# Kernel optimization log

Measured on AMD Instinct MI355X. Metric: run time of the kernel, lower is better.

The kernel has to match this reference:

```python
import jax, jax.numpy as jnp
import numpy as np

B, N, L = 4, 16, 2048
E = 32768
CH = (64, 128, 128, 128)
EPS = 1e-5


def setup_inputs() -> dict:
    key = jax.random.key(0)
    ks = jax.random.split(key, 6)
    x = jax.random.normal(ks[0], (B, N, CH[0], L), jnp.float32)
    edge_index = jax.random.randint(ks[1], (2, E), 0, L, dtype=jnp.int64)

    def xavier(k, fi, fo):
        std = (2.0 / (fi + fo)) ** 0.5
        return jax.random.normal(k, (fi, fo), jnp.float32) * std

    W1 = xavier(ks[2], CH[0], CH[1])
    W2 = xavier(ks[3], 2 * CH[1], CH[2])
    W3 = xavier(ks[4], 2 * CH[2], CH[3])
    return dict(
        x=x, edge_index=edge_index,
        W1=W1, b1=jnp.zeros((CH[1],), jnp.float32),
        W2=W2, b2=jnp.zeros((CH[2],), jnp.float32),
        W3=W3, b3=jnp.zeros((CH[3],), jnp.float32),
        g1=jnp.ones((2 * CH[1],), jnp.float32), be1=jnp.zeros((2 * CH[1],), jnp.float32),
        g2=jnp.ones((2 * CH[2],), jnp.float32), be2=jnp.zeros((2 * CH[2],), jnp.float32),
        g3=jnp.ones((2 * CH[3],), jnp.float32), be3=jnp.zeros((2 * CH[3],), jnp.float32),
    )


def _gcn_norm(edge_index, l):
    # PyG gcn_norm with improved=True: self loops get weight 2, sym normalization
    src, dst = edge_index[0], edge_index[1]
    loop = jnp.arange(l)
    src_f = jnp.concatenate([src, loop])
    dst_f = jnp.concatenate([dst, loop])
    w = jnp.concatenate([jnp.ones((src.shape[0],), jnp.float32),
                         2.0 * jnp.ones((l,), jnp.float32)])
    deg = jax.ops.segment_sum(w, dst_f, num_segments=l)
    dinv = jnp.where(deg > 0, jax.lax.rsqrt(deg), 0.0)
    return src_f, dst_f, dinv[src_f] * w * dinv[dst_f]


def _gcn(h, W, bias, src, dst, norm):
    # h: [G, l, c_in] -> [G, l, c_out];  out[i] = sum_{j->i} norm_ij * (h_j @ W) + b
    hW = jnp.einsum('glc,cf->glf', h, W)
    msg = hW[:, src, :] * norm[None, :, None]
    out = jnp.zeros_like(hW).at[:, dst, :].add(msg)
    return out + bias


def _block(h, W, bias, g, beta, src, dst, norm, b, n, l):
    # h: [b, n, l, c_in]
    a = _gcn(h.reshape(b * n, l, h.shape[-1]), W, bias, src, dst, norm)
    a = a.reshape(b, n, l, -1)
    amax = a.max(axis=1, keepdims=True)
    a = jnp.concatenate([a, jnp.broadcast_to(amax, a.shape)], axis=-1)  # [b,n,l,2c]
    # BatchNorm1d training stats over (b, n, l) per channel (biased var)
    mean = a.mean(axis=(0, 1, 2))
    var = a.var(axis=(0, 1, 2))
    return jax.nn.relu((a - mean) * jax.lax.rsqrt(var + EPS) * g + beta)


def reference(x, edge_index, W1, b1, W2, b2, W3, b3, g1, be1, g2, be2, g3, be3):
    b, n, c, l = x.shape
    h = jnp.transpose(x, (0, 1, 3, 2))  # [b, n, l, c] node-major
    src, dst, norm = _gcn_norm(edge_index, l)
    h = _block(h, W1, b1, g1, be1, src, dst, norm, b, n, l)
    h = _block(h, W2, b2, g2, be2, src, dst, norm, b, n, l)
    h = _block(h, W3, b3, g3, be3, src, dst, norm, b, n, l)
    # match torch output layout [b*n, 2*channels[3], l]
    return jnp.transpose(h.reshape(b * n, l, -1), (0, 2, 1))
```

## Files before the change

kernel.cpp:

```cpp
#include <hip/hip_runtime.h>
#include <hip/hip_bf16.h>
#include <cstddef>
#include <cstdint>

#define BB 4
#define NN 16
#define GG 64
#define LL 2048
#define EE 32768
#define EF (EE + LL)
#define C0 64
#define CC 256
#define EPS 1e-5f

typedef __bf16 bf16x8 __attribute__((ext_vector_type(8)));
typedef __bf16 bf16x4 __attribute__((ext_vector_type(4)));
typedef __bf16 bf16x2 __attribute__((ext_vector_type(2)));
typedef float f32x4 __attribute__((ext_vector_type(4)));

struct __align__(8) Edge { int col; float val; };


__global__ void detect_kernel(const int* __restrict__ ei, int* __restrict__ flag) {
    int t = threadIdx.x;
    int bad = 0;
    for (int i = t; i < 256; i += 64) bad |= (ei[2 * i + 1] != 0) ? 1 : 0;
    int any = __any(bad);
    if (t == 0) *flag = any ? 0 : 1;
}

__global__ void convert_kernel(const void* __restrict__ ei, const int* __restrict__ flag,
                               int* __restrict__ e32) {
    int i = blockIdx.x * 256 + threadIdx.x;
    if (i >= 2 * EE) return;
    int v;
    if (*flag)
        v = (int)((const long long*)ei)[i];
    else
        v = ((const int*)ei)[i];
    e32[i] = v;
}

__global__ void initdeg_kernel(float* __restrict__ deg, int* __restrict__ cnt) {
    int i = blockIdx.x * 256 + threadIdx.x;
    if (i < LL) { deg[i] = 2.0f; cnt[i] = 1; }
}

__global__ void deg_kernel(const int* __restrict__ e32, float* __restrict__ deg,
                           int* __restrict__ cnt) {
    int e = blockIdx.x * 256 + threadIdx.x;
    if (e >= EE) return;
    int d = e32[EE + e];
    atomicAdd(&deg[d], 1.0f);
    atomicAdd(&cnt[d], 1);
}

__global__ void dinv_kernel(const float* __restrict__ deg, float* __restrict__ dinv) {
    int i = blockIdx.x * 256 + threadIdx.x;
    if (i < LL) dinv[i] = rsqrtf(deg[i]);
}

__global__ void scan_kernel(const int* __restrict__ cnt, int* __restrict__ rowptr,
                            int* __restrict__ cursor) {
    __shared__ int part[256];
    int t = threadIdx.x;
    int base = t * 8;
    int loc[8];
    int s = 0;
#pragma unroll
    for (int j = 0; j < 8; ++j) { loc[j] = s; s += cnt[base + j]; }
    part[t] = s;
    __syncthreads();
    if (t == 0) {
        int run = 0;
        for (int i = 0; i < 256; ++i) { int v = part[i]; part[i] = run; run += v; }
    }
    __syncthreads();
    int off = part[t];
#pragma unroll
    for (int j = 0; j < 8; ++j) {
        int rp = off + loc[j];
        rowptr[base + j] = rp;
        cursor[base + j] = rp;
    }
    if (t == 255) rowptr[LL] = off + s;
}

__global__ void fill_kernel(const int* __restrict__ e32, const float* __restrict__ dinv,
                            int* __restrict__ cursor, Edge* __restrict__ edges) {
    int idx = blockIdx.x * 256 + threadIdx.x;
    if (idx >= EF) return;
    int s, d; float w;
    if (idx < EE) {
        s = e32[idx]; d = e32[EE + idx];
        w = dinv[s] * dinv[d];
    } else {
        int i = idx - EE;
        s = i; d = i;
        w = 2.0f * dinv[i] * dinv[i];
    }
    int pos = atomicAdd(&cursor[d], 1);
    edges[pos].col = s;
    edges[pos].val = w;
}


__global__ void prep_w(const float* __restrict__ W, __bf16* __restrict__ Wf, int K) {
    int t = blockIdx.x * 256 + threadIdx.x;
    int total = (K / 32) * 8 * 64;
    if (t >= total) return;
    int lane = t & 63;
    int rest = t >> 6;
    int n16 = rest & 7;
    int ks = rest >> 3;
    int col = n16 * 16 + (lane & 15);
    int k0 = ks * 32 + (lane >> 4) * 8;
    bf16x8 v;
#pragma unroll
    for (int j = 0; j < 8; ++j) v[j] = (__bf16)W[(size_t)(k0 + j) * 128 + col];
    *(bf16x8*)(Wf + (size_t)t * 8) = v;
}


__global__ void transpose_x(const float* __restrict__ x, float* __restrict__ h) {
    __shared__ float t[32][33];
    int g = blockIdx.z, c0 = blockIdx.y * 32, l0 = blockIdx.x * 32;
    int tx = threadIdx.x, ty = threadIdx.y;
    const float* xp = x + ((size_t)g * C0 + c0) * LL + l0;
#pragma unroll
    for (int i = ty; i < 32; i += 8) t[i][tx] = xp[(size_t)i * LL + tx];
    __syncthreads();
    float* hp = h + ((size_t)g * LL + l0) * C0 + c0;
#pragma unroll
    for (int i = ty; i < 32; i += 8) hp[(size_t)i * C0 + tx] = t[tx][i];
}


template <int K, bool BN>
__global__ __launch_bounds__(256) void gemm_mfma(const float* __restrict__ A0,
                                                 const float* __restrict__ amax,
                                                 const float* __restrict__ scb,
                                                 const __bf16* __restrict__ Wf,
                                                 __bf16* __restrict__ hw) {
    const int g = blockIdx.y;
    const int l0 = blockIdx.x * 64;
    const int tid = threadIdx.x;
    const int wid = tid >> 6;
    const int lane = tid & 63;
    __shared__ __align__(16) __bf16 As[64 * 64];

    f32x4 acc[8];
#pragma unroll
    for (int nf = 0; nf < 8; ++nf) acc[nf] = (f32x4){0.f, 0.f, 0.f, 0.f};

    const int AS = BN ? 128 : 64;

    for (int kt = 0; kt < K / 64; ++kt) {
#pragma unroll
        for (int it = 0; it < 4; ++it) {
            int f4 = tid + it * 256;
            int row = f4 >> 4;
            int kq = (f4 & 15) * 4;
            int gk = kt * 64 + kq;
            float4 v;
            if constexpr (BN) {
                if (gk < 128)
                    v = *(const float4*)(A0 + ((size_t)g * LL + l0 + row) * 128 + gk);
                else
                    v = *(const float4*)(amax + ((size_t)(g >> 4) * LL + l0 + row) * 128 + (gk - 128));
                float4 s = *(const float4*)(scb + gk);
                float4 b = *(const float4*)(scb + 256 + gk);
                v.x = fmaxf(fmaf(v.x, s.x, b.x), 0.f);
                v.y = fmaxf(fmaf(v.y, s.y, b.y), 0.f);
                v.z = fmaxf(fmaf(v.z, s.z, b.z), 0.f);
                v.w = fmaxf(fmaf(v.w, s.w, b.w), 0.f);
            } else {
                v = *(const float4*)(A0 + ((size_t)g * LL + l0 + row) * 64 + gk);
            }
            int sidx = row * 64 + (kq ^ ((row & 7) << 3));
            bf16x4 pv = {(__bf16)v.x, (__bf16)v.y, (__bf16)v.z, (__bf16)v.w};
            *(bf16x4*)(&As[sidx]) = pv;
        }
        __syncthreads();
#pragma unroll
        for (int ks2 = 0; ks2 < 2; ++ks2) {
            const int row = wid * 16 + (lane & 15);
            const int kk = ks2 * 32 + (lane >> 4) * 8;
            bf16x8 af = *(const bf16x8*)(&As[row * 64 + (kk ^ ((row & 7) << 3))]);
            const int ksg = kt * 2 + ks2;
            const __bf16* wp = Wf + (size_t)ksg * 8 * 512 + lane * 8;
#pragma unroll
            for (int nf = 0; nf < 8; ++nf) {
                bf16x8 bfr = *(const bf16x8*)(wp + nf * 512);
                acc[nf] = __builtin_amdgcn_mfma_f32_16x16x32_bf16(af, bfr, acc[nf], 0, 0, 0);
            }
        }
        __syncthreads();
    }
    __bf16* op = hw + ((size_t)g * LL + l0) * 128;
#pragma unroll
    for (int nf = 0; nf < 8; ++nf) {
        int col = nf * 16 + (lane & 15);
#pragma unroll
        for (int j = 0; j < 4; ++j) {
            int row = wid * 16 + (lane >> 4) * 4 + j;
            op[(size_t)row * 128 + col] = (__bf16)acc[nf][j];
        }
    }
}


__global__ __launch_bounds__(256) void agg_kernel(const __bf16* __restrict__ hw,
                                                  const float* __restrict__ bias,
                                                  const int* __restrict__ rowptr,
                                                  const Edge* __restrict__ edges,
                                                  float* __restrict__ aout) {
    const int lane = threadIdx.x & 63;
    int node = blockIdx.x * 4 + (threadIdx.x >> 6);
    node = __builtin_amdgcn_readfirstlane(node);
    const int g = node >> 11, l = node & (LL - 1);
    const __bf16* __restrict__ base = hw + (size_t)g * LL * 128;
    const int j0 = rowptr[l];
    const int deg = rowptr[l + 1] - j0;

    float2 acc = *(const float2*)(bias + 2 * lane);

    for (int d0 = 0; d0 < deg; d0 += 64) {
        const int cnt = min(64, deg - d0);
        Edge e;
        e.col = 0; e.val = 0.0f;
        if (lane < cnt) e = edges[j0 + d0 + lane];
        int d = 0;
        for (; d + 4 <= cnt; d += 4) {
            int c0 = __shfl(e.col, d);
            int c1 = __shfl(e.col, d + 1);
            int c2 = __shfl(e.col, d + 2);
            int c3 = __shfl(e.col, d + 3);
            float w0 = __shfl(e.val, d);
            float w1 = __shfl(e.val, d + 1);
            float w2 = __shfl(e.val, d + 2);
            float w3 = __shfl(e.val, d + 3);
            bf16x2 v0 = *(const bf16x2*)(base + (size_t)c0 * 128 + 2 * lane);
            bf16x2 v1 = *(const bf16x2*)(base + (size_t)c1 * 128 + 2 * lane);
            bf16x2 v2 = *(const bf16x2*)(base + (size_t)c2 * 128 + 2 * lane);
            bf16x2 v3 = *(const bf16x2*)(base + (size_t)c3 * 128 + 2 * lane);
            acc.x = fmaf(w0, (float)v0[0], acc.x); acc.y = fmaf(w0, (float)v0[1], acc.y);
            acc.x = fmaf(w1, (float)v1[0], acc.x); acc.y = fmaf(w1, (float)v1[1], acc.y);
            acc.x = fmaf(w2, (float)v2[0], acc.x); acc.y = fmaf(w2, (float)v2[1], acc.y);
            acc.x = fmaf(w3, (float)v3[0], acc.x); acc.y = fmaf(w3, (float)v3[1], acc.y);
        }
        for (; d < cnt; ++d) {
            int c = __shfl(e.col, d);
            float wv = __shfl(e.val, d);
            bf16x2 v = *(const bf16x2*)(base + (size_t)c * 128 + 2 * lane);
            acc.x = fmaf(wv, (float)v[0], acc.x);
            acc.y = fmaf(wv, (float)v[1], acc.y);
        }
    }
    *(float2*)(aout + (size_t)node * 128 + 2 * lane) = acc;
}


__global__ void maxstats_kernel(const float* __restrict__ a, float* __restrict__ amax,
                                float* __restrict__ sums, float* __restrict__ sumsq) {
    int bb = blockIdx.x >> 7;
    int lt = blockIdx.x & 127;
    int l0 = lt * 16;
    int f = threadIdx.x;
    float s = 0.f, ss = 0.f, sa = 0.f, ssa = 0.f;
    for (int li = 0; li < 16; ++li) {
        int l = l0 + li;
        float m = -3.402823466e38f;
#pragma unroll
        for (int n = 0; n < NN; ++n) {
            float v = a[(((size_t)(bb * NN + n) * LL + l) * 128) + f];
            m = fmaxf(m, v);
            s += v;
            ss = fmaf(v, v, ss);
        }
        amax[((size_t)bb * LL + l) * 128 + f] = m;
        sa += m;
        ssa = fmaf(m, m, ssa);
    }
    atomicAdd(&sums[f], s);
    atomicAdd(&sumsq[f], ss);
    atomicAdd(&sums[128 + f], sa);
    atomicAdd(&sumsq[128 + f], ssa);
}

__global__ void bnfinal_kernel(const float* __restrict__ sums, const float* __restrict__ sumsq,
                               const float* __restrict__ gamma, const float* __restrict__ beta,
                               float* __restrict__ scb) {
    int f = threadIdx.x;
    float cntv = (f < 128) ? (float)(BB * NN * LL) : (float)(BB * LL);
    float mean = sums[f] / cntv;
    float var = sumsq[f] / cntv - mean * mean;
    float s = gamma[f] * rsqrtf(var + EPS);
    scb[f] = s;
    scb[256 + f] = beta[f] - mean * s;
}


__global__ void transpose_norm_out(const float* __restrict__ a, const float* __restrict__ amax,
                                   const float* __restrict__ scb, float* __restrict__ out) {
    __shared__ float t[32][33];
    int g = blockIdx.z, f0 = blockIdx.y * 32, l0 = blockIdx.x * 32;
    int tx = threadIdx.x, ty = threadIdx.y;
    int f = f0 + tx;
    float s = scb[f], b = scb[256 + f];
#pragma unroll
    for (int i = ty; i < 32; i += 8) {
        int l = l0 + i;
        float v;
        if (f0 < 128)
            v = a[((size_t)g * LL + l) * 128 + f];
        else
            v = amax[((size_t)(g >> 4) * LL + l) * 128 + (f - 128)];
        t[i][tx] = fmaxf(fmaf(v, s, b), 0.f);
    }
    __syncthreads();
    float* op = out + ((size_t)g * CC + f0) * LL + l0;
#pragma unroll
    for (int i = ty; i < 32; i += 8) op[(size_t)i * LL + tx] = t[tx][i];
}


extern "C" void kernel_launch(void* const* d_in, const int* in_sizes, int n_in,
                              void* d_out, int out_size, void* d_ws, size_t ws_size,
                              hipStream_t stream) {
    const float* x = (const float*)d_in[0];
    const void* ei = d_in[1];
    const float* W[3] = {(const float*)d_in[2], (const float*)d_in[4], (const float*)d_in[6]};
    const float* bia[3] = {(const float*)d_in[3], (const float*)d_in[5], (const float*)d_in[7]};
    const float* gam[3] = {(const float*)d_in[8], (const float*)d_in[10], (const float*)d_in[12]};
    const float* bet[3] = {(const float*)d_in[9], (const float*)d_in[11], (const float*)d_in[13]};
    float* out = (float*)d_out;

    char* w = (char*)d_ws;
    float* h0   = (float*)w;  w += (size_t)GG * LL * C0 * 4;
    float* a    = (float*)w;  w += (size_t)GG * LL * 128 * 4;
    __bf16* hw  = (__bf16*)w; w += (size_t)GG * LL * 128 * 2;
    float* amax = (float*)w;  w += (size_t)BB * LL * 128 * 4;
    __bf16* Wf[3];
    Wf[0] = (__bf16*)w; w += 65536 * 2;
    Wf[1] = (__bf16*)w; w += 65536 * 2;
    Wf[2] = (__bf16*)w; w += 65536 * 2;
    int*   e32   = (int*)w;    w += (size_t)2 * EE * 4;
    float* deg   = (float*)w;  w += LL * 4;
    int*   cnt   = (int*)w;    w += LL * 4;
    int*   rowptr= (int*)w;    w += (LL + 4) * 4;
    int*   cursor= (int*)w;    w += LL * 4;
    Edge*  edges = (Edge*)w;   w += (size_t)EF * 8;
    float* dinv  = (float*)w;  w += LL * 4;
    float* sums  = (float*)w;  w += 256 * 4;
    float* sumsq = (float*)w;  w += 256 * 4;
    float* scb   = (float*)w;  w += 512 * 4;
    int*   flag  = (int*)w;    w += 256;

    detect_kernel<<<1, 64, 0, stream>>>((const int*)ei, flag);
    convert_kernel<<<(2 * EE + 255) / 256, 256, 0, stream>>>(ei, flag, e32);
    initdeg_kernel<<<(LL + 255) / 256, 256, 0, stream>>>(deg, cnt);
    deg_kernel<<<(EE + 255) / 256, 256, 0, stream>>>(e32, deg, cnt);
    dinv_kernel<<<(LL + 255) / 256, 256, 0, stream>>>(deg, dinv);
    scan_kernel<<<1, 256, 0, stream>>>(cnt, rowptr, cursor);
    fill_kernel<<<(EF + 255) / 256, 256, 0, stream>>>(e32, dinv, cursor, edges);

    prep_w<<<(1024 + 255) / 256, 256, 0, stream>>>(W[0], Wf[0], 64);
    prep_w<<<(4096 + 255) / 256, 256, 0, stream>>>(W[1], Wf[1], 256);
    prep_w<<<(4096 + 255) / 256, 256, 0, stream>>>(W[2], Wf[2], 256);

    transpose_x<<<dim3(LL / 32, C0 / 32, GG), dim3(32, 8), 0, stream>>>(x, h0);

    gemm_mfma<64, false><<<dim3(LL / 64, GG), 256, 0, stream>>>(h0, amax, scb, Wf[0], hw);
    agg_kernel<<<GG * LL / 4, 256, 0, stream>>>(hw, bia[0], rowptr, edges, a);
    hipMemsetAsync(sums, 0, 2 * 256 * 4, stream);
    maxstats_kernel<<<BB * (LL / 16), 128, 0, stream>>>(a, amax, sums, sumsq);
    bnfinal_kernel<<<1, 256, 0, stream>>>(sums, sumsq, gam[0], bet[0], scb);

    gemm_mfma<256, true><<<dim3(LL / 64, GG), 256, 0, stream>>>(a, amax, scb, Wf[1], hw);
    agg_kernel<<<GG * LL / 4, 256, 0, stream>>>(hw, bia[1], rowptr, edges, a);
    hipMemsetAsync(sums, 0, 2 * 256 * 4, stream);
    maxstats_kernel<<<BB * (LL / 16), 128, 0, stream>>>(a, amax, sums, sumsq);
    bnfinal_kernel<<<1, 256, 0, stream>>>(sums, sumsq, gam[1], bet[1], scb);

    gemm_mfma<256, true><<<dim3(LL / 64, GG), 256, 0, stream>>>(a, amax, scb, Wf[2], hw);
    agg_kernel<<<GG * LL / 4, 256, 0, stream>>>(hw, bia[2], rowptr, edges, a);
    hipMemsetAsync(sums, 0, 2 * 256 * 4, stream);
    maxstats_kernel<<<BB * (LL / 16), 128, 0, stream>>>(a, amax, sums, sumsq);
    bnfinal_kernel<<<1, 256, 0, stream>>>(sums, sumsq, gam[2], bet[2], scb);

    transpose_norm_out<<<dim3(LL / 32, CC / 32, GG), dim3(32, 8), 0, stream>>>(a, amax, scb, out);
}
```

Baseline: 597.4 us.

## Vectorize aggregation gathers, fuse setup kernels, drop memsets, enlarge output transpose tiles

The aggregation kernel now has each 16-lane group gather a full 128-channel row with 16-byte bf16x8 loads, four neighbours per step, then reduce the partial sums across the groups with xor shuffles. Several small setup kernels are merged (convert+initdeg, scan+dinv), and the per-layer memsets are removed: the stats buffers are zeroed in the prep kernel and by bnfinal after it reads them. The output transpose moves to 64x64 tiles. This trims launch overhead and gather instruction count, at the cost of extra cross-lane reductions and wasted work when a node's degree is not a multiple of four.

```diff
diff --git a/kernel.cpp b/kernel.cpp
--- a/kernel.cpp
+++ b/kernel.cpp
@@ -29,21 +29,20 @@
     if (t == 0) *flag = any ? 0 : 1;
 }
 
-__global__ void convert_kernel(const void* __restrict__ ei, const int* __restrict__ flag,
-                               int* __restrict__ e32) {
+__global__ void prep_init_kernel(const void* __restrict__ ei, const int* __restrict__ flag,
+                                 int* __restrict__ e32, float* __restrict__ deg,
+                                 int* __restrict__ cnt, float* __restrict__ sums) {
     int i = blockIdx.x * 256 + threadIdx.x;
-    if (i >= 2 * EE) return;
-    int v;
-    if (*flag)
-        v = (int)((const long long*)ei)[i];
-    else
-        v = ((const int*)ei)[i];
-    e32[i] = v;
-}
-
-__global__ void initdeg_kernel(float* __restrict__ deg, int* __restrict__ cnt) {
-    int i = blockIdx.x * 256 + threadIdx.x;
+    if (i < 2 * EE) {
+        int v;
+        if (*flag)
+            v = (int)((const long long*)ei)[i];
+        else
+            v = ((const int*)ei)[i];
+        e32[i] = v;
+    }
     if (i < LL) { deg[i] = 2.0f; cnt[i] = 1; }
+    if (i < 512) sums[i] = 0.0f;
 }
 
 __global__ void deg_kernel(const int* __restrict__ e32, float* __restrict__ deg,
@@ -55,20 +54,19 @@
     atomicAdd(&cnt[d], 1);
 }
 
-__global__ void dinv_kernel(const float* __restrict__ deg, float* __restrict__ dinv) {
-    int i = blockIdx.x * 256 + threadIdx.x;
-    if (i < LL) dinv[i] = rsqrtf(deg[i]);
-}
-
-__global__ void scan_kernel(const int* __restrict__ cnt, int* __restrict__ rowptr,
-                            int* __restrict__ cursor) {
+__global__ void scan_dinv_kernel(const int* __restrict__ cnt, const float* __restrict__ deg,
+                                 int* __restrict__ rowptr, int* __restrict__ cursor,
+                                 float* __restrict__ dinv) {
     __shared__ int part[256];
     int t = threadIdx.x;
     int base = t * 8;
     int loc[8];
     int s = 0;
 #pragma unroll
-    for (int j = 0; j < 8; ++j) { loc[j] = s; s += cnt[base + j]; }
+    for (int j = 0; j < 8; ++j) {
+        loc[j] = s; s += cnt[base + j];
+        dinv[base + j] = rsqrtf(deg[base + j]);
+    }
     part[t] = s;
     __syncthreads();
     if (t == 0) {
@@ -152,8 +150,6 @@
     f32x4 acc[8];
 #pragma unroll
     for (int nf = 0; nf < 8; ++nf) acc[nf] = (f32x4){0.f, 0.f, 0.f, 0.f};
-
-    const int AS = BN ? 128 : 64;
 
     for (int kt = 0; kt < K / 64; ++kt) {
 #pragma unroll
@@ -216,14 +212,18 @@
                                                   const Edge* __restrict__ edges,
                                                   float* __restrict__ aout) {
     const int lane = threadIdx.x & 63;
+    const int grp = lane >> 4;
+    const int ch16 = lane & 15;
     int node = blockIdx.x * 4 + (threadIdx.x >> 6);
     node = __builtin_amdgcn_readfirstlane(node);
     const int g = node >> 11, l = node & (LL - 1);
-    const __bf16* __restrict__ base = hw + (size_t)g * LL * 128;
+    const __bf16* __restrict__ base = hw + (size_t)g * LL * 128 + ch16 * 8;
     const int j0 = rowptr[l];
     const int deg = rowptr[l + 1] - j0;
 
-    float2 acc = *(const float2*)(bias + 2 * lane);
+    float acc[8];
+#pragma unroll
+    for (int j = 0; j < 8; ++j) acc[j] = 0.0f;
 
     for (int d0 = 0; d0 < deg; d0 += 64) {
         const int cnt = min(64, deg - d0);
@@ -231,33 +231,39 @@
         e.col = 0; e.val = 0.0f;
         if (lane < cnt) e = edges[j0 + d0 + lane];
         int d = 0;
-        for (; d + 4 <= cnt; d += 4) {
-            int c0 = __shfl(e.col, d);
-            int c1 = __shfl(e.col, d + 1);
-            int c2 = __shfl(e.col, d + 2);
-            int c3 = __shfl(e.col, d + 3);
-            float w0 = __shfl(e.val, d);
-            float w1 = __shfl(e.val, d + 1);
-            float w2 = __shfl(e.val, d + 2);
-            float w3 = __shfl(e.val, d + 3);
-            bf16x2 v0 = *(const bf16x2*)(base + (size_t)c0 * 128 + 2 * lane);
-            bf16x2 v1 = *(const bf16x2*)(base + (size_t)c1 * 128 + 2 * lane);
-            bf16x2 v2 = *(const bf16x2*)(base + (size_t)c2 * 128 + 2 * lane);
-            bf16x2 v3 = *(const bf16x2*)(base + (size_t)c3 * 128 + 2 * lane);
-            acc.x = fmaf(w0, (float)v0[0], acc.x); acc.y = fmaf(w0, (float)v0[1], acc.y);
-            acc.x = fmaf(w1, (float)v1[0], acc.x); acc.y = fmaf(w1, (float)v1[1], acc.y);
-            acc.x = fmaf(w2, (float)v2[0], acc.x); acc.y = fmaf(w2, (float)v2[1], acc.y);
-            acc.x = fmaf(w3, (float)v3[0], acc.x); acc.y = fmaf(w3, (float)v3[1], acc.y);
-        }
-        for (; d < cnt; ++d) {
-            int c = __shfl(e.col, d);
-            float wv = __shfl(e.val, d);
-            bf16x2 v = *(const bf16x2*)(base + (size_t)c * 128 + 2 * lane);
-            acc.x = fmaf(wv, (float)v[0], acc.x);
-            acc.y = fmaf(wv, (float)v[1], acc.y);
-        }
-    }
-    *(float2*)(aout + (size_t)node * 128 + 2 * lane) = acc;
+        for (; d + 8 <= cnt; d += 8) {
+            int i1 = d + grp, i2 = d + 4 + grp;
+            int c1 = __shfl(e.col, i1); float w1 = __shfl(e.val, i1);
+            int c2 = __shfl(e.col, i2); float w2 = __shfl(e.val, i2);
+            bf16x8 v1 = *(const bf16x8*)(base + (size_t)c1 * 128);
+            bf16x8 v2 = *(const bf16x8*)(base + (size_t)c2 * 128);
+#pragma unroll
+            for (int j = 0; j < 8; ++j) acc[j] = fmaf(w1, (float)v1[j], acc[j]);
+#pragma unroll
+            for (int j = 0; j < 8; ++j) acc[j] = fmaf(w2, (float)v2[j], acc[j]);
+        }
+        for (; d < cnt; d += 4) {
+            int i1 = d + grp;
+            int c1 = __shfl(e.col, i1); float w1 = __shfl(e.val, i1);
+            bf16x8 v1 = *(const bf16x8*)(base + (size_t)c1 * 128);
+#pragma unroll
+            for (int j = 0; j < 8; ++j) acc[j] = fmaf(w1, (float)v1[j], acc[j]);
+        }
+    }
+#pragma unroll
+    for (int j = 0; j < 8; ++j) {
+        acc[j] += __shfl_xor(acc[j], 16);
+        acc[j] += __shfl_xor(acc[j], 32);
+    }
+    if (grp == 0) {
+        float4 b0 = *(const float4*)(bias + ch16 * 8);
+        float4 b1 = *(const float4*)(bias + ch16 * 8 + 4);
+        float4 s0 = make_float4(acc[0] + b0.x, acc[1] + b0.y, acc[2] + b0.z, acc[3] + b0.w);
+        float4 s1 = make_float4(acc[4] + b1.x, acc[5] + b1.y, acc[6] + b1.z, acc[7] + b1.w);
+        float* op = aout + (size_t)node * 128 + ch16 * 8;
+        *(float4*)op = s0;
+        *(float4*)(op + 4) = s1;
+    }
 }
 
 
@@ -288,7 +294,7 @@
     atomicAdd(&sumsq[128 + f], ssa);
 }
 
-__global__ void bnfinal_kernel(const float* __restrict__ sums, const float* __restrict__ sumsq,
+__global__ void bnfinal_kernel(float* __restrict__ sums, float* __restrict__ sumsq,
                                const float* __restrict__ gamma, const float* __restrict__ beta,
                                float* __restrict__ scb) {
     int f = threadIdx.x;
@@ -298,18 +304,20 @@
     float s = gamma[f] * rsqrtf(var + EPS);
     scb[f] = s;
     scb[256 + f] = beta[f] - mean * s;
+    sums[f] = 0.0f;
+    sumsq[f] = 0.0f;
 }
 
 
 __global__ void transpose_norm_out(const float* __restrict__ a, const float* __restrict__ amax,
                                    const float* __restrict__ scb, float* __restrict__ out) {
-    __shared__ float t[32][33];
-    int g = blockIdx.z, f0 = blockIdx.y * 32, l0 = blockIdx.x * 32;
+    __shared__ float t[64][65];
+    int g = blockIdx.z, f0 = blockIdx.y * 64, l0 = blockIdx.x * 64;
     int tx = threadIdx.x, ty = threadIdx.y;
     int f = f0 + tx;
     float s = scb[f], b = scb[256 + f];
 #pragma unroll
-    for (int i = ty; i < 32; i += 8) {
+    for (int i = ty; i < 64; i += 8) {
         int l = l0 + i;
         float v;
         if (f0 < 128)
@@ -321,7 +329,7 @@
     __syncthreads();
     float* op = out + ((size_t)g * CC + f0) * LL + l0;
 #pragma unroll
-    for (int i = ty; i < 32; i += 8) op[(size_t)i * LL + tx] = t[tx][i];
+    for (int i = ty; i < 64; i += 8) op[(size_t)i * LL + tx] = t[tx][i];
 }
 
 
@@ -358,11 +366,9 @@
     int*   flag  = (int*)w;    w += 256;
 
     detect_kernel<<<1, 64, 0, stream>>>((const int*)ei, flag);
-    convert_kernel<<<(2 * EE + 255) / 256, 256, 0, stream>>>(ei, flag, e32);
-    initdeg_kernel<<<(LL + 255) / 256, 256, 0, stream>>>(deg, cnt);
+    prep_init_kernel<<<(2 * EE + 255) / 256, 256, 0, stream>>>(ei, flag, e32, deg, cnt, sums);
     deg_kernel<<<(EE + 255) / 256, 256, 0, stream>>>(e32, deg, cnt);
-    dinv_kernel<<<(LL + 255) / 256, 256, 0, stream>>>(deg, dinv);
-    scan_kernel<<<1, 256, 0, stream>>>(cnt, rowptr, cursor);
+    scan_dinv_kernel<<<1, 256, 0, stream>>>(cnt, deg, rowptr, cursor, dinv);
     fill_kernel<<<(EF + 255) / 256, 256, 0, stream>>>(e32, dinv, cursor, edges);
 
     prep_w<<<(1024 + 255) / 256, 256, 0, stream>>>(W[0], Wf[0], 64);
@@ -373,21 +379,18 @@
 
     gemm_mfma<64, false><<<dim3(LL / 64, GG), 256, 0, stream>>>(h0, amax, scb, Wf[0], hw);
     agg_kernel<<<GG * LL / 4, 256, 0, stream>>>(hw, bia[0], rowptr, edges, a);
-    hipMemsetAsync(sums, 0, 2 * 256 * 4, stream);
     maxstats_kernel<<<BB * (LL / 16), 128, 0, stream>>>(a, amax, sums, sumsq);
     bnfinal_kernel<<<1, 256, 0, stream>>>(sums, sumsq, gam[0], bet[0], scb);
 
     gemm_mfma<256, true><<<dim3(LL / 64, GG), 256, 0, stream>>>(a, amax, scb, Wf[1], hw);
     agg_kernel<<<GG * LL / 4, 256, 0, stream>>>(hw, bia[1], rowptr, edges, a);
-    hipMemsetAsync(sums, 0, 2 * 256 * 4, stream);
     maxstats_kernel<<<BB * (LL / 16), 128, 0, stream>>>(a, amax, sums, sumsq);
     bnfinal_kernel<<<1, 256, 0, stream>>>(sums, sumsq, gam[1], bet[1], scb);
 
     gemm_mfma<256, true><<<dim3(LL / 64, GG), 256, 0, stream>>>(a, amax, scb, Wf[2], hw);
     agg_kernel<<<GG * LL / 4, 256, 0, stream>>>(hw, bia[2], rowptr, edges, a);
-    hipMemsetAsync(sums, 0, 2 * 256 * 4, stream);
     maxstats_kernel<<<BB * (LL / 16), 128, 0, stream>>>(a, amax, sums, sumsq);
     bnfinal_kernel<<<1, 256, 0, stream>>>(sums, sumsq, gam[2], bet[2], scb);
 
-    transpose_norm_out<<<dim3(LL / 32, CC / 32, GG), dim3(32, 8), 0, stream>>>(a, amax, scb, out);
-}
+    transpose_norm_out<<<dim3(LL / 64, CC / 64, GG), dim3(64, 8), 0, stream>>>(a, amax, scb, out);
+}
```

After: 561.4 us. 1.06x faster.
